# Optimization experiments

Measured on AMD Instinct MI355X. Metric: run time of the kernel, lower is better.

## Reference

```python
import jax, jax.numpy as jnp
import numpy as np

N = 50000      # nodes
E = 800000     # edges (avg degree 16)
D_IN, D_H, D_OUT = 128, 128, 64


def setup_inputs() -> dict:
    key = jax.random.key(0)
    ks = jax.random.split(key, 12)
    s = 0.05  # weight init scale
    return {
        "x": jax.random.normal(ks[0], (N, D_IN), jnp.float32),
        "edge_index": jax.random.randint(ks[1], (2, E), 0, N, dtype=jnp.int64),
        "Wl0": jax.random.normal(ks[2], (D_H, D_IN), jnp.float32) * s,
        "bl0": jax.random.normal(ks[3], (D_H,), jnp.float32) * s,
        "Wr0": jax.random.normal(ks[4], (D_H, D_IN), jnp.float32) * s,
        "Wl1": jax.random.normal(ks[5], (D_H, D_H), jnp.float32) * s,
        "bl1": jax.random.normal(ks[6], (D_H,), jnp.float32) * s,
        "Wr1": jax.random.normal(ks[7], (D_H, D_H), jnp.float32) * s,
        "Wl2": jax.random.normal(ks[8], (D_OUT, D_H), jnp.float32) * s,
        "bl2": jax.random.normal(ks[9], (D_OUT,), jnp.float32) * s,
        "Wr2": jax.random.normal(ks[10], (D_OUT, D_H), jnp.float32) * s,
    }


def _sage_layer(h, src, dst, Wl, bl, Wr):
    # mean aggregation over incoming neighbors: out[i] = mean_{j in N(i)} h[j]
    n = h.shape[0]
    agg = jax.ops.segment_sum(h[src], dst, num_segments=n)          # [N, D]
    deg = jax.ops.segment_sum(jnp.ones((src.shape[0],), h.dtype), dst,
                              num_segments=n)                        # [N]
    mean = agg / jnp.maximum(deg, 1.0)[:, None]  # empty rows -> 0, matches torch_sparse
    # lin_l(agg) + lin_r(self); lin_r has no bias in PyG SAGEConv
    return mean @ Wl.T + bl + h @ Wr.T


def reference(x, edge_index, Wl0, bl0, Wr0, Wl1, bl1, Wr1, Wl2, bl2, Wr2):
    src, dst = edge_index[1], edge_index[0]  # adj row = dst, col = src
    h = jax.nn.relu(_sage_layer(x, src, dst, Wl0, bl0, Wr0))
    h = jax.nn.relu(_sage_layer(h, src, dst, Wl1, bl1, Wr1))
    h = _sage_layer(h, src, dst, Wl2, bl2, Wr2)
    return jax.nn.log_softmax(h, axis=1)
```

## Files before the change

kernel.cpp:

```cpp
#include <hip/hip_runtime.h>
#include <hip/hip_bf16.h>


typedef __attribute__((ext_vector_type(8))) short bf16x8;
typedef __attribute__((ext_vector_type(4))) float f32x4;

#define NPB 128
#define BCAP 2560
#define EPB 8192
#define EPT 32
#define CPAD 16

__device__ __forceinline__ unsigned short f2bf(float f) {
    unsigned int u = __builtin_bit_cast(unsigned int, f);
    u += 0x7fffu + ((u >> 16) & 1u);
    return (unsigned short)(u >> 16);
}
__device__ __forceinline__ float bf2f(unsigned int bits16) {
    return __builtin_bit_cast(float, bits16 << 16);
}


__global__ __launch_bounds__(256) void dist_cast_kernel(const int* __restrict__ dst,
                                                        const int* __restrict__ srcv,
                                                        int* __restrict__ gcnt,
                                                        unsigned int* __restrict__ staging,
                                                        int E, int NBc, int DB, int XB,
                                                        const float* __restrict__ x,
                                                        unsigned short* __restrict__ xbf,
                                                        const float* p0, const float* p1,
                                                        const float* p2, const float* p3,
                                                        const float* p4, const float* p5,
                                                        unsigned short* __restrict__ wbf) {
    __shared__ unsigned int stage[EPB];
    __shared__ int hist[400];
    __shared__ int lstart[400];
    __shared__ int gbase[400];
    __shared__ int scanbuf[256];
    int bid = blockIdx.x;
    int t = threadIdx.x;

    if (bid >= DB && bid < DB + XB) {
        int base = (bid - DB) * 256 + t;
        int stride = XB * 256;
        const float2* x2 = (const float2*)x;
        unsigned int* xo = (unsigned int*)xbf;
#pragma unroll
        for (int k = 0; k < 4; ++k) {
            int idx = base + k * stride;
            float2 v = x2[idx];
            xo[idx] = (unsigned int)f2bf(v.x) | ((unsigned int)f2bf(v.y) << 16);
        }
        return;
    }
    if (bid >= DB + XB) {
        int w = (bid - DB - XB) * 256 + t;
        if (w < 40960) {
            const float* src;
            int local;
            if      (w < 8192)  { src = p0; local = w; }
            else if (w < 16384) { src = p1; local = w - 8192; }
            else if (w < 24576) { src = p2; local = w - 16384; }
            else if (w < 32768) { src = p3; local = w - 24576; }
            else if (w < 36864) { src = p4; local = w - 32768; }
            else                { src = p5; local = w - 36864; }
            float2 v = ((const float2*)src)[local];
            unsigned int p = (unsigned int)f2bf(v.x) | ((unsigned int)f2bf(v.y) << 16);
            ((unsigned int*)wbf)[w] = p;
        }
        return;
    }

    int e0 = bid * EPB;
    unsigned int w[EPT];

    for (int b = t; b < NBc + 1; b += 256) hist[b] = 0;
    __syncthreads();

#pragma unroll
    for (int i = 0; i < EPT; ++i) {
        int e = e0 + i * 256 + t;
        unsigned int word = 0xFFFFFFFFu;
        if (e < E) word = ((unsigned int)dst[e] << 16) | (unsigned int)srcv[e];
        w[i] = word;
        int b = (int)(word >> 23); if (b > NBc) b = NBc;
        atomicAdd(&hist[b], 1);
    }
    __syncthreads();

    int b0 = 2 * t, b1 = 2 * t + 1;
    int h0 = (b0 <= NBc) ? hist[b0] : 0;
    int h1 = (b1 <= NBc) ? hist[b1] : 0;
    int pair = h0 + h1;
    scanbuf[t] = pair;
    __syncthreads();
    for (int off = 1; off < 256; off <<= 1) {
        int v = (t >= off) ? scanbuf[t - off] : 0;
        __syncthreads();
        scanbuf[t] += v;
        __syncthreads();
    }
    int excl = scanbuf[t] - pair;
    if (b0 <= NBc) lstart[b0] = excl;
    if (b1 <= NBc) lstart[b1] = excl + h0;
    __syncthreads();

    for (int b = t; b < NBc; b += 256) {
        int h = hist[b];
        gbase[b] = h ? atomicAdd(&gcnt[b * CPAD], h) : 0;
    }
    for (int b = t; b < NBc + 1; b += 256) hist[b] = lstart[b];
    __syncthreads();

#pragma unroll
    for (int i = 0; i < EPT; ++i) {
        unsigned int word = w[i];
        int b = (int)(word >> 23); if (b > NBc) b = NBc;
        int p = atomicAdd(&hist[b], 1);
        stage[p] = word;
    }
    __syncthreads();

    int total = lstart[NBc];
    for (int i = t; i < total; i += 256) {
        unsigned int word = stage[i];
        int b = (int)(word >> 23);
        int gpos = gbase[b] + (i - lstart[b]);
        staging[(size_t)b * BCAP + gpos] = word;
    }
}


template<int GY>
__device__ __forceinline__ void gemm_body(int mb, int y,
                                          const unsigned short* __restrict__ H,
                                          const unsigned short* __restrict__ Wl,
                                          const unsigned short* __restrict__ Wr,
                                          unsigned short* __restrict__ Cl,
                                          unsigned short* __restrict__ Cr, int N) {
    __shared__ unsigned short clds[4 * 32 * 68];
    const int halfY = GY >> 1;
    const int ldc = GY * 32;
    int wave = threadIdx.x >> 6;
    int lane = threadIdx.x & 63;
    int l15 = lane & 15, quad = lane >> 4;
    bool isL = y < halfY;
    const unsigned short* W = isL ? Wl : Wr;
    unsigned short* Cp = isL ? Cl : Cr;
    int yy = isL ? y : y - halfY;
    int wrow0 = yy * 64;
    int col0 = yy * 64;
    int m0 = mb * 128 + wave * 32;

    int r0 = m0 + l15;      if (r0 > N - 1) r0 = N - 1;
    int r1 = m0 + 16 + l15; if (r1 > N - 1) r1 = N - 1;
    const bf16x8* A0 = (const bf16x8*)(H + (size_t)r0 * 128);
    const bf16x8* A1 = (const bf16x8*)(H + (size_t)r1 * 128);

    f32x4 acc[2][4] = {};
#pragma unroll
    for (int ks = 0; ks < 4; ++ks) {
        int vidx = ks * 4 + quad;
        bf16x8 a0 = A0[vidx];
        bf16x8 a1 = A1[vidx];
#pragma unroll
        for (int j = 0; j < 4; ++j) {
            const bf16x8* B = (const bf16x8*)(W + (size_t)(wrow0 + j * 16 + l15) * 128);
            bf16x8 b = B[vidx];
            acc[0][j] = __builtin_amdgcn_mfma_f32_16x16x32_bf16(a0, b, acc[0][j], 0, 0, 0);
            acc[1][j] = __builtin_amdgcn_mfma_f32_16x16x32_bf16(a1, b, acc[1][j], 0, 0, 0);
        }
    }

    unsigned short* slice = clds + wave * (32 * 68);
#pragma unroll
    for (int i = 0; i < 2; ++i)
#pragma unroll
        for (int j = 0; j < 4; ++j)
#pragma unroll
            for (int r = 0; r < 4; ++r)
                slice[(i * 16 + quad * 4 + r) * 68 + j * 16 + l15] = f2bf(acc[i][j][r]);
    __syncthreads();

    int rlo = lane >> 3, j8 = lane & 7;
#pragma unroll
    for (int pass = 0; pass < 4; ++pass) {
        int row_local = pass * 8 + rlo;
        const unsigned short* p = slice + row_local * 68 + j8 * 8;
        unsigned long long lo = *(const unsigned long long*)(p);
        unsigned long long hi = *(const unsigned long long*)(p + 4);
        int row = m0 + row_local;
        if (row < N) {
            unsigned long long* q = (unsigned long long*)(Cp + (size_t)row * ldc + col0 + j8 * 8);
            q[0] = lo;
            q[1] = hi;
        }
    }
}


__global__ __launch_bounds__(256) void build_gemm_kernel(const unsigned int* __restrict__ staging,
                                                         const int* __restrict__ gcnt,
                                                         int* __restrict__ row_ptr,
                                                         int* __restrict__ adj, int N, int NBc,
                                                         int gemmRows,
                                                         const unsigned short* __restrict__ H,
                                                         const unsigned short* __restrict__ Wl,
                                                         const unsigned short* __restrict__ Wr,
                                                         unsigned short* __restrict__ Cl,
                                                         unsigned short* __restrict__ Cr) {
    __shared__ int hist[NPB];
    __shared__ int scn[NPB];
    __shared__ int wsum[4];
    int bid = blockIdx.x;
    int t = threadIdx.x;

    if (bid >= NBc) {
        int gid = bid - NBc;
        int mb = gid % gemmRows;
        int yy = gid / gemmRows;
        gemm_body<4>(mb, yy, H, Wl, Wr, Cl, Cr, N);
        return;
    }

    int b = bid;
    int n0 = b * NPB;
    int nb = N - n0; if (nb > NPB) nb = NPB;
    int ec = gcnt[b * CPAD];
    const unsigned int* st = staging + (size_t)b * BCAP;

    int a = 0;
    for (int j = t; j < b; j += 256) a += gcnt[j * CPAD];
#pragma unroll
    for (int off = 32; off; off >>= 1) a += __shfl_xor(a, off);
    if ((t & 63) == 0) wsum[t >> 6] = a;
    if (t < NPB) hist[t] = 0;
    __syncthreads();
    int bb = wsum[0] + wsum[1] + wsum[2] + wsum[3];

    for (int i = t; i < ec; i += 256)
        atomicAdd(&hist[(st[i] >> 16) & (NPB - 1)], 1);
    __syncthreads();

    int v = (t < NPB) ? hist[t] : 0;
    if (t < NPB) scn[t] = v;
    __syncthreads();
    for (int off = 1; off < NPB; off <<= 1) {
        int u = (t >= off && t < NPB) ? scn[t - off] : 0;
        __syncthreads();
        if (t < NPB) scn[t] += u;
        __syncthreads();
    }
    if (t < NPB) hist[t] = scn[t] - v;
    if (t < nb) row_ptr[n0 + t] = bb + (scn[t] - v);
    if (b == NBc - 1 && t == 0) row_ptr[N] = bb + ec;
    __syncthreads();

    for (int i = t; i < ec; i += 256) {
        unsigned int pk = st[i];
        int p = atomicAdd(&hist[(pk >> 16) & (NPB - 1)], 1);
        adj[bb + p] = (int)(pk & 0xffffu);
    }
}


template<int GY>
__global__ __launch_bounds__(256) void gemm_mfma_kernel(const unsigned short* __restrict__ H,
                                                        const unsigned short* __restrict__ Wl,
                                                        const unsigned short* __restrict__ Wr,
                                                        unsigned short* __restrict__ Cl,
                                                        unsigned short* __restrict__ Cr,
                                                        int N) {
    gemm_body<GY>(blockIdx.x, blockIdx.y, Wl ? H : H, Wl, Wr, Cl, Cr, N);
}


__global__ __launch_bounds__(256) void agg_relu_kernel(const unsigned short* __restrict__ Cl,
                                                       const unsigned short* __restrict__ Cr,
                                                       const int* __restrict__ row_ptr,
                                                       const int* __restrict__ adj,
                                                       const float* __restrict__ bias,
                                                       unsigned short* __restrict__ hout, int N) {
    int pr = (int)((blockIdx.x * blockDim.x + threadIdx.x) >> 6);
    int lane = threadIdx.x & 63;
    int nodeA = pr * 2;
    if (nodeA >= N) return;
    int nodeB = nodeA + 1;
    bool hasB = nodeB < N;
    int g = lane >> 4, c = lane & 15;
    int begA = row_ptr[nodeA], endA = row_ptr[nodeA + 1];
    int begB = hasB ? row_ptr[nodeB] : 0;
    int endB = hasB ? row_ptr[nodeB + 1] : 0;
    float pA[8] = {}, pB[8] = {};

    int cntA = endA - begA; if (cntA > 64) cntA = 64;
    int cntB = endB - begB; if (cntB > 64) cntB = 64;
    int idxA = (cntA > 0) ? adj[begA + (lane < cntA ? lane : cntA - 1)] : 0;
    int idxB = (cntB > 0) ? adj[begB + (lane < cntB ? lane : cntB - 1)] : 0;
    int c1A = cntA - 1, c1B = cntB - 1;
    int mx = cntA > cntB ? cntA : cntB;
    for (int i = 0; i < mx; i += 16) {
        bool doA = i < cntA, doB = i < cntB;
        bf16x8 vA[4], vB[4];
        float mA[4], mB[4];
        if (doA) {
#pragma unroll
            for (int s = 0; s < 4; ++s) {
                int tt = i + s * 4 + g;
                int src = __shfl(idxA, tt > c1A ? c1A : tt);
                mA[s] = tt < cntA ? 1.f : 0.f;
                vA[s] = ((const bf16x8*)(Cl + (size_t)src * 128))[c];
            }
        }
        if (doB) {
#pragma unroll
            for (int s = 0; s < 4; ++s) {
                int tt = i + s * 4 + g;
                int src = __shfl(idxB, tt > c1B ? c1B : tt);
                mB[s] = tt < cntB ? 1.f : 0.f;
                vB[s] = ((const bf16x8*)(Cl + (size_t)src * 128))[c];
            }
        }
        if (doA) {
#pragma unroll
            for (int s = 0; s < 4; ++s)
#pragma unroll
                for (int k = 0; k < 8; ++k)
                    pA[k] += mA[s] * bf2f((unsigned short)vA[s][k]);
        }
        if (doB) {
#pragma unroll
            for (int s = 0; s < 4; ++s)
#pragma unroll
                for (int k = 0; k < 8; ++k)
                    pB[k] += mB[s] * bf2f((unsigned short)vB[s][k]);
        }
    }
    for (int e = begA + 64; e < endA; e += 64) {
        int cnt = endA - e; if (cnt > 64) cnt = 64;
        int idx = adj[e + (lane < cnt ? lane : cnt - 1)];
        int c1 = cnt - 1;
        for (int i = 0; i < cnt; i += 16) {
#pragma unroll
            for (int s = 0; s < 4; ++s) {
                int tt = i + s * 4 + g;
                int src = __shfl(idx, tt > c1 ? c1 : tt);
                float m = tt < cnt ? 1.f : 0.f;
                bf16x8 v = ((const bf16x8*)(Cl + (size_t)src * 128))[c];
#pragma unroll
                for (int k = 0; k < 8; ++k)
                    pA[k] += m * bf2f((unsigned short)v[k]);
            }
        }
    }
    for (int e = begB + 64; e < endB; e += 64) {
        int cnt = endB - e; if (cnt > 64) cnt = 64;
        int idx = adj[e + (lane < cnt ? lane : cnt - 1)];
        int c1 = cnt - 1;
        for (int i = 0; i < cnt; i += 16) {
#pragma unroll
            for (int s = 0; s < 4; ++s) {
                int tt = i + s * 4 + g;
                int src = __shfl(idx, tt > c1 ? c1 : tt);
                float m = tt < cnt ? 1.f : 0.f;
                bf16x8 v = ((const bf16x8*)(Cl + (size_t)src * 128))[c];
#pragma unroll
                for (int k = 0; k < 8; ++k)
                    pB[k] += m * bf2f((unsigned short)v[k]);
            }
        }
    }

#pragma unroll
    for (int k = 0; k < 8; ++k) {
        pA[k] += __shfl_xor(pA[k], 16);
        pA[k] += __shfl_xor(pA[k], 32);
        pB[k] += __shfl_xor(pB[k], 16);
        pB[k] += __shfl_xor(pB[k], 32);
    }

    int degA = endA - begA, degB = endB - begB;
    float invA = 1.0f / (float)(degA > 1 ? degA : 1);
    float invB = 1.0f / (float)(degB > 1 ? degB : 1);
    bf16x8 svA = ((const bf16x8*)(Cr + (size_t)nodeA * 128))[c];
    bf16x8 svB = hasB ? ((const bf16x8*)(Cr + (size_t)nodeB * 128))[c] : svA;
    float4 b0 = ((const float4*)bias)[2 * c];
    float4 b1 = ((const float4*)bias)[2 * c + 1];
    float bb[8] = {b0.x, b0.y, b0.z, b0.w, b1.x, b1.y, b1.z, b1.w};
    bf16x8 oA, oB;
#pragma unroll
    for (int k = 0; k < 8; ++k) {
        oA[k] = (short)f2bf(fmaxf(pA[k] * invA + bb[k] + bf2f((unsigned short)svA[k]), 0.f));
        oB[k] = (short)f2bf(fmaxf(pB[k] * invB + bb[k] + bf2f((unsigned short)svB[k]), 0.f));
    }
    if (g == 0)
        ((bf16x8*)(hout + (size_t)nodeA * 128))[c] = oA;
    else if (g == 1 && hasB)
        ((bf16x8*)(hout + (size_t)nodeB * 128))[c] = oB;
}


__global__ __launch_bounds__(256) void final_kernel(const unsigned short* __restrict__ Cl2,
                                                    const unsigned short* __restrict__ Cr2,
                                                    const int* __restrict__ row_ptr,
                                                    const int* __restrict__ adj,
                                                    const float* __restrict__ bias,
                                                    float* __restrict__ out, int N) {
    int pr = (int)((blockIdx.x * blockDim.x + threadIdx.x) >> 6);
    int lane = threadIdx.x & 63;
    int nodeA = pr * 2;
    if (nodeA >= N) return;
    int nodeB = nodeA + 1;
    bool hasB = nodeB < N;
    int g = lane >> 3, c = lane & 7;
    int begA = row_ptr[nodeA], endA = row_ptr[nodeA + 1];
    int begB = hasB ? row_ptr[nodeB] : 0;
    int endB = hasB ? row_ptr[nodeB + 1] : 0;
    float pA[8] = {}, pB[8] = {};

    int cntA = endA - begA; if (cntA > 64) cntA = 64;
    int cntB = endB - begB; if (cntB > 64) cntB = 64;
    int idxA = (cntA > 0) ? adj[begA + (lane < cntA ? lane : cntA - 1)] : 0;
    int idxB = (cntB > 0) ? adj[begB + (lane < cntB ? lane : cntB - 1)] : 0;
    int c1A = cntA - 1, c1B = cntB - 1;
    int mx = cntA > cntB ? cntA : cntB;
    for (int i = 0; i < mx; i += 16) {
        bool doA = i < cntA, doB = i < cntB;
        bf16x8 vA[2], vB[2];
        float mA[2], mB[2];
        if (doA) {
#pragma unroll
            for (int s = 0; s < 2; ++s) {
                int tt = i + s * 8 + g;
                int src = __shfl(idxA, tt > c1A ? c1A : tt);
                mA[s] = tt < cntA ? 1.f : 0.f;
                vA[s] = ((const bf16x8*)(Cl2 + (size_t)src * 64))[c];
            }
        }
        if (doB) {
#pragma unroll
            for (int s = 0; s < 2; ++s) {
                int tt = i + s * 8 + g;
                int src = __shfl(idxB, tt > c1B ? c1B : tt);
                mB[s] = tt < cntB ? 1.f : 0.f;
                vB[s] = ((const bf16x8*)(Cl2 + (size_t)src * 64))[c];
            }
        }
        if (doA) {
#pragma unroll
            for (int s = 0; s < 2; ++s)
#pragma unroll
                for (int k = 0; k < 8; ++k)
                    pA[k] += mA[s] * bf2f((unsigned short)vA[s][k]);
        }
        if (doB) {
#pragma unroll
            for (int s = 0; s < 2; ++s)
#pragma unroll
                for (int k = 0; k < 8; ++k)
                    pB[k] += mB[s] * bf2f((unsigned short)vB[s][k]);
        }
    }
    for (int e = begA + 64; e < endA; e += 64) {
        int cnt = endA - e; if (cnt > 64) cnt = 64;
        int idx = adj[e + (lane < cnt ? lane : cnt - 1)];
        int c1 = cnt - 1;
        for (int i = 0; i < cnt; i += 16) {
#pragma unroll
            for (int s = 0; s < 2; ++s) {
                int tt = i + s * 8 + g;
                int src = __shfl(idx, tt > c1 ? c1 : tt);
                float m = tt < cnt ? 1.f : 0.f;
                bf16x8 v = ((const bf16x8*)(Cl2 + (size_t)src * 64))[c];
#pragma unroll
                for (int k = 0; k < 8; ++k)
                    pA[k] += m * bf2f((unsigned short)v[k]);
            }
        }
    }
    for (int e = begB + 64; e < endB; e += 64) {
        int cnt = endB - e; if (cnt > 64) cnt = 64;
        int idx = adj[e + (lane < cnt ? lane : cnt - 1)];
        int c1 = cnt - 1;
        for (int i = 0; i < cnt; i += 16) {
#pragma unroll
            for (int s = 0; s < 2; ++s) {
                int tt = i + s * 8 + g;
                int src = __shfl(idx, tt > c1 ? c1 : tt);
                float m = tt < cnt ? 1.f : 0.f;
                bf16x8 v = ((const bf16x8*)(Cl2 + (size_t)src * 64))[c];
#pragma unroll
                for (int k = 0; k < 8; ++k)
                    pB[k] += m * bf2f((unsigned short)v[k]);
            }
        }
    }

#pragma unroll
    for (int k = 0; k < 8; ++k) {
        pA[k] += __shfl_xor(pA[k], 8);
        pA[k] += __shfl_xor(pA[k], 16);
        pA[k] += __shfl_xor(pA[k], 32);
        pB[k] += __shfl_xor(pB[k], 8);
        pB[k] += __shfl_xor(pB[k], 16);
        pB[k] += __shfl_xor(pB[k], 32);
    }

    int degA = endA - begA, degB = endB - begB;
    float invA = 1.0f / (float)(degA > 1 ? degA : 1);
    float invB = 1.0f / (float)(degB > 1 ? degB : 1);
    bf16x8 svA = ((const bf16x8*)(Cr2 + (size_t)nodeA * 64))[c];
    bf16x8 svB = hasB ? ((const bf16x8*)(Cr2 + (size_t)nodeB * 64))[c] : svA;
    float4 b0 = ((const float4*)bias)[2 * c];
    float4 b1 = ((const float4*)bias)[2 * c + 1];
    float bb[8] = {b0.x, b0.y, b0.z, b0.w, b1.x, b1.y, b1.z, b1.w};
    float uA[8], uB[8];
#pragma unroll
    for (int k = 0; k < 8; ++k) {
        uA[k] = pA[k] * invA + bb[k] + bf2f((unsigned short)svA[k]);
        uB[k] = pB[k] * invB + bb[k] + bf2f((unsigned short)svB[k]);
    }

    float mA_ = uA[0], mB_ = uB[0];
#pragma unroll
    for (int k = 1; k < 8; ++k) { mA_ = fmaxf(mA_, uA[k]); mB_ = fmaxf(mB_, uB[k]); }
#pragma unroll
    for (int off = 1; off < 8; off <<= 1) {
        mA_ = fmaxf(mA_, __shfl_xor(mA_, off));
        mB_ = fmaxf(mB_, __shfl_xor(mB_, off));
    }
    float seA = 0.f, seB = 0.f;
#pragma unroll
    for (int k = 0; k < 8; ++k) { seA += __expf(uA[k] - mA_); seB += __expf(uB[k] - mB_); }
#pragma unroll
    for (int off = 1; off < 8; off <<= 1) {
        seA += __shfl_xor(seA, off);
        seB += __shfl_xor(seB, off);
    }
    float lsA = __logf(seA), lsB = __logf(seB);

    if (g == 0) {
        float4 o0 = {uA[0] - mA_ - lsA, uA[1] - mA_ - lsA, uA[2] - mA_ - lsA, uA[3] - mA_ - lsA};
        float4 o1 = {uA[4] - mA_ - lsA, uA[5] - mA_ - lsA, uA[6] - mA_ - lsA, uA[7] - mA_ - lsA};
        ((float4*)(out + (size_t)nodeA * 64))[2 * c] = o0;
        ((float4*)(out + (size_t)nodeA * 64))[2 * c + 1] = o1;
    } else if (g == 1 && hasB) {
        float4 o0 = {uB[0] - mB_ - lsB, uB[1] - mB_ - lsB, uB[2] - mB_ - lsB, uB[3] - mB_ - lsB};
        float4 o1 = {uB[4] - mB_ - lsB, uB[5] - mB_ - lsB, uB[6] - mB_ - lsB, uB[7] - mB_ - lsB};
        ((float4*)(out + (size_t)nodeB * 64))[2 * c] = o0;
        ((float4*)(out + (size_t)nodeB * 64))[2 * c + 1] = o1;
    }
}


extern "C" void kernel_launch(void* const* d_in, const int* in_sizes, int n_in,
                              void* d_out, int out_size, void* d_ws, size_t ws_size,
                              hipStream_t stream) {
    const float* x   = (const float*)d_in[0];
    const int*   ei  = (const int*)d_in[1];
    const float* Wl0 = (const float*)d_in[2];
    const float* bl0 = (const float*)d_in[3];
    const float* Wr0 = (const float*)d_in[4];
    const float* Wl1 = (const float*)d_in[5];
    const float* bl1 = (const float*)d_in[6];
    const float* Wr1 = (const float*)d_in[7];
    const float* Wl2 = (const float*)d_in[8];
    const float* bl2 = (const float*)d_in[9];
    const float* Wr2 = (const float*)d_in[10];
    float* out = (float*)d_out;

    const int N  = in_sizes[0] / 128;
    const int E  = in_sizes[1] / 2;
    const int NB = (N + NPB - 1) / NPB;

    char* ws = (char*)d_ws;
    auto alloc = [&](size_t bytes) {
        char* p = ws;
        ws += (bytes + 255) & ~(size_t)255;
        return p;
    };
    int*   row_ptr    = (int*)alloc((size_t)(N + 1) * 4);
    int*   adj        = (int*)alloc((size_t)E * 4);
    int*   gcnt      = (int*)alloc((size_t)NB * CPAD * 4);
    unsigned int* staging = (unsigned int*)alloc((size_t)NB * BCAP * 4);
    unsigned short* xbf = (unsigned short*)alloc((size_t)N * 128 * 2);
    unsigned short* wbf = (unsigned short*)alloc((size_t)81920 * 2);
    unsigned short* Cl  = (unsigned short*)alloc((size_t)N * 128 * 2);
    unsigned short* Cr  = (unsigned short*)alloc((size_t)N * 128 * 2);
    unsigned short* hA  = (unsigned short*)alloc((size_t)N * 128 * 2);
    unsigned short* hB  = (unsigned short*)alloc((size_t)N * 128 * 2);

    const int* dstp = ei;
    const int* srcp = ei + E;

    unsigned short* wl0 = wbf;
    unsigned short* wr0 = wbf + 16384;
    unsigned short* wl1 = wbf + 32768;
    unsigned short* wr1 = wbf + 49152;
    unsigned short* wl2 = wbf + 65536;
    unsigned short* wr2 = wbf + 73728;

    dim3 blk(256);
    int DB = (E + EPB - 1) / EPB;
    int XB = (N * 64) / (256 * 4);
    int gemmRows = (N + 127) / 128;
    int pairBlocks = (((N + 1) / 2) * 64 + 255) / 256;

    hipMemsetAsync(gcnt, 0, (size_t)NB * CPAD * 4, stream);
    dist_cast_kernel<<<DB + XB + 160, blk, 0, stream>>>(dstp, srcp, gcnt, staging, E, NB,
                                                        DB, XB, x, xbf,
                                                        Wl0, Wr0, Wl1, Wr1, Wl2, Wr2, wbf);
    build_gemm_kernel<<<NB + gemmRows * 4, blk, 0, stream>>>(staging, gcnt, row_ptr, adj,
                                                             N, NB, gemmRows, xbf, wl0, wr0,
                                                             Cl, Cr);
    agg_relu_kernel<<<pairBlocks, blk, 0, stream>>>(Cl, Cr, row_ptr, adj, bl0, hA, N);
    gemm_mfma_kernel<4><<<dim3(gemmRows, 4), blk, 0, stream>>>(hA, wl1, wr1, Cl, Cr, N);
    agg_relu_kernel<<<pairBlocks, blk, 0, stream>>>(Cl, Cr, row_ptr, adj, bl1, hB, N);
    gemm_mfma_kernel<2><<<dim3(gemmRows, 2), blk, 0, stream>>>(hB, wl2, wr2, Cl, Cr, N);
    final_kernel<<<pairBlocks, blk, 0, stream>>>(Cl, Cr, row_ptr, adj, bl2, out, N);
}
```

Baseline: 273.3 us.

## Store 128-wide features in column-sliced layout and aggregate per slice

The GEMM epilogue for layers 0 and 1 now writes the neighbor-projected features in a sliced layout of eight [N,16] column slices instead of row-major [N,128]. A new aggregation kernel assigns each block one slice, and each lane pair gathers 32-byte rows per neighbor. This shrinks the per-slice gather working set so it stays cache-resident and improves L2 locality of random neighbor reads. The following GEMM reads its A operand from the sliced layout. It trades coalesced wide row reads for more blocks, eight passes over adjacency, and an extra __syncthreads in the GEMM.

```diff
diff --git a/kernel.cpp b/kernel.cpp
--- a/kernel.cpp
+++ b/kernel.cpp
@@ -131,7 +131,7 @@
 }
 
 
-template<int GY>
+template<int GY, int ASL, int CSL>
 __device__ __forceinline__ void gemm_body(int mb, int y,
                                           const unsigned short* __restrict__ H,
                                           const unsigned short* __restrict__ Wl,
@@ -154,15 +154,20 @@
 
     int r0 = m0 + l15;      if (r0 > N - 1) r0 = N - 1;
     int r1 = m0 + 16 + l15; if (r1 > N - 1) r1 = N - 1;
-    const bf16x8* A0 = (const bf16x8*)(H + (size_t)r0 * 128);
-    const bf16x8* A1 = (const bf16x8*)(H + (size_t)r1 * 128);
 
     f32x4 acc[2][4] = {};
 #pragma unroll
     for (int ks = 0; ks < 4; ++ks) {
         int vidx = ks * 4 + quad;
-        bf16x8 a0 = A0[vidx];
-        bf16x8 a1 = A1[vidx];
+        bf16x8 a0, a1;
+        if constexpr (ASL) {
+            const unsigned short* base = H + (size_t)(vidx >> 1) * N * 16 + (vidx & 1) * 8;
+            a0 = *(const bf16x8*)(base + (size_t)r0 * 16);
+            a1 = *(const bf16x8*)(base + (size_t)r1 * 16);
+        } else {
+            a0 = ((const bf16x8*)(H + (size_t)r0 * 128))[vidx];
+            a1 = ((const bf16x8*)(H + (size_t)r1 * 128))[vidx];
+        }
 #pragma unroll
         for (int j = 0; j < 4; ++j) {
             const bf16x8* B = (const bf16x8*)(W + (size_t)(wrow0 + j * 16 + l15) * 128);
@@ -182,20 +187,40 @@
                 slice[(i * 16 + quad * 4 + r) * 68 + j * 16 + l15] = f2bf(acc[i][j][r]);
     __syncthreads();
 
-    int rlo = lane >> 3, j8 = lane & 7;
-#pragma unroll
-    for (int pass = 0; pass < 4; ++pass) {
-        int row_local = pass * 8 + rlo;
-        const unsigned short* p = slice + row_local * 68 + j8 * 8;
-        unsigned long long lo = *(const unsigned long long*)(p);
-        unsigned long long hi = *(const unsigned long long*)(p + 4);
-        int row = m0 + row_local;
+    if (CSL && isL) {
+        int nodeLocal = lane >> 1, hf = lane & 1;
+        int row = m0 + nodeLocal;
+        int s0 = col0 >> 4;
         if (row < N) {
-            unsigned long long* q = (unsigned long long*)(Cp + (size_t)row * ldc + col0 + j8 * 8);
-            q[0] = lo;
-            q[1] = hi;
-        }
-    }
+#pragma unroll
+            for (int sl = 0; sl < 4; ++sl) {
+                const unsigned short* p = slice + nodeLocal * 68 + sl * 16 + hf * 8;
+                unsigned long long lo = *(const unsigned long long*)(p);
+                unsigned long long hi = *(const unsigned long long*)(p + 4);
+                unsigned long long* q =
+                    (unsigned long long*)(Cl + ((size_t)(s0 + sl) * N + row) * 16 + hf * 8);
+                q[0] = lo;
+                q[1] = hi;
+            }
+        }
+    } else {
+        int rlo = lane >> 3, j8 = lane & 7;
+#pragma unroll
+        for (int pass = 0; pass < 4; ++pass) {
+            int row_local = pass * 8 + rlo;
+            const unsigned short* p = slice + row_local * 68 + j8 * 8;
+            unsigned long long lo = *(const unsigned long long*)(p);
+            unsigned long long hi = *(const unsigned long long*)(p + 4);
+            int row = m0 + row_local;
+            if (row < N) {
+                unsigned long long* q =
+                    (unsigned long long*)(Cp + (size_t)row * ldc + col0 + j8 * 8);
+                q[0] = lo;
+                q[1] = hi;
+            }
+        }
+    }
+    __syncthreads();
 }
 
 
@@ -217,9 +242,7 @@
 
     if (bid >= NBc) {
         int gid = bid - NBc;
-        int mb = gid % gemmRows;
-        int yy = gid / gemmRows;
-        gemm_body<4>(mb, yy, H, Wl, Wr, Cl, Cr, N);
+        gemm_body<4, 0, 1>(gid % gemmRows, gid / gemmRows, H, Wl, Wr, Cl, Cr, N);
         return;
     }
 
@@ -264,139 +287,69 @@
 }
 
 
-template<int GY>
+template<int GY, int ASL, int CSL>
 __global__ __launch_bounds__(256) void gemm_mfma_kernel(const unsigned short* __restrict__ H,
                                                         const unsigned short* __restrict__ Wl,
                                                         const unsigned short* __restrict__ Wr,
                                                         unsigned short* __restrict__ Cl,
                                                         unsigned short* __restrict__ Cr,
                                                         int N) {
-    gemm_body<GY>(blockIdx.x, blockIdx.y, Wl ? H : H, Wl, Wr, Cl, Cr, N);
-}
-
-
-__global__ __launch_bounds__(256) void agg_relu_kernel(const unsigned short* __restrict__ Cl,
-                                                       const unsigned short* __restrict__ Cr,
-                                                       const int* __restrict__ row_ptr,
-                                                       const int* __restrict__ adj,
-                                                       const float* __restrict__ bias,
-                                                       unsigned short* __restrict__ hout, int N) {
-    int pr = (int)((blockIdx.x * blockDim.x + threadIdx.x) >> 6);
+    gemm_body<GY, ASL, CSL>(blockIdx.x, blockIdx.y, H, Wl, Wr, Cl, Cr, N);
+}
+
+
+__global__ __launch_bounds__(256) void agg_sliced_kernel(const unsigned short* __restrict__ Cls,
+                                                         const unsigned short* __restrict__ Cr,
+                                                         const int* __restrict__ row_ptr,
+                                                         const int* __restrict__ adj,
+                                                         const float* __restrict__ bias,
+                                                         unsigned short* __restrict__ houts,
+                                                         int N) {
+    int s = blockIdx.x & 7;
+    int nb = blockIdx.x >> 3;
+    int wave = threadIdx.x >> 6;
     int lane = threadIdx.x & 63;
-    int nodeA = pr * 2;
-    if (nodeA >= N) return;
-    int nodeB = nodeA + 1;
-    bool hasB = nodeB < N;
-    int g = lane >> 4, c = lane & 15;
-    int begA = row_ptr[nodeA], endA = row_ptr[nodeA + 1];
-    int begB = hasB ? row_ptr[nodeB] : 0;
-    int endB = hasB ? row_ptr[nodeB + 1] : 0;
-    float pA[8] = {}, pB[8] = {};
-
-    int cntA = endA - begA; if (cntA > 64) cntA = 64;
-    int cntB = endB - begB; if (cntB > 64) cntB = 64;
-    int idxA = (cntA > 0) ? adj[begA + (lane < cntA ? lane : cntA - 1)] : 0;
-    int idxB = (cntB > 0) ? adj[begB + (lane < cntB ? lane : cntB - 1)] : 0;
-    int c1A = cntA - 1, c1B = cntB - 1;
-    int mx = cntA > cntB ? cntA : cntB;
-    for (int i = 0; i < mx; i += 16) {
-        bool doA = i < cntA, doB = i < cntB;
-        bf16x8 vA[4], vB[4];
-        float mA[4], mB[4];
-        if (doA) {
-#pragma unroll
-            for (int s = 0; s < 4; ++s) {
-                int tt = i + s * 4 + g;
-                int src = __shfl(idxA, tt > c1A ? c1A : tt);
-                mA[s] = tt < cntA ? 1.f : 0.f;
-                vA[s] = ((const bf16x8*)(Cl + (size_t)src * 128))[c];
-            }
-        }
-        if (doB) {
-#pragma unroll
-            for (int s = 0; s < 4; ++s) {
-                int tt = i + s * 4 + g;
-                int src = __shfl(idxB, tt > c1B ? c1B : tt);
-                mB[s] = tt < cntB ? 1.f : 0.f;
-                vB[s] = ((const bf16x8*)(Cl + (size_t)src * 128))[c];
-            }
-        }
-        if (doA) {
-#pragma unroll
-            for (int s = 0; s < 4; ++s)
-#pragma unroll
-                for (int k = 0; k < 8; ++k)
-                    pA[k] += mA[s] * bf2f((unsigned short)vA[s][k]);
-        }
-        if (doB) {
-#pragma unroll
-            for (int s = 0; s < 4; ++s)
-#pragma unroll
-                for (int k = 0; k < 8; ++k)
-                    pB[k] += mB[s] * bf2f((unsigned short)vB[s][k]);
-        }
-    }
-    for (int e = begA + 64; e < endA; e += 64) {
-        int cnt = endA - e; if (cnt > 64) cnt = 64;
-        int idx = adj[e + (lane < cnt ? lane : cnt - 1)];
-        int c1 = cnt - 1;
-        for (int i = 0; i < cnt; i += 16) {
-#pragma unroll
-            for (int s = 0; s < 4; ++s) {
-                int tt = i + s * 4 + g;
-                int src = __shfl(idx, tt > c1 ? c1 : tt);
-                float m = tt < cnt ? 1.f : 0.f;
-                bf16x8 v = ((const bf16x8*)(Cl + (size_t)src * 128))[c];
-#pragma unroll
-                for (int k = 0; k < 8; ++k)
-                    pA[k] += m * bf2f((unsigned short)v[k]);
-            }
-        }
-    }
-    for (int e = begB + 64; e < endB; e += 64) {
-        int cnt = endB - e; if (cnt > 64) cnt = 64;
-        int idx = adj[e + (lane < cnt ? lane : cnt - 1)];
-        int c1 = cnt - 1;
-        for (int i = 0; i < cnt; i += 16) {
-#pragma unroll
-            for (int s = 0; s < 4; ++s) {
-                int tt = i + s * 4 + g;
-                int src = __shfl(idx, tt > c1 ? c1 : tt);
-                float m = tt < cnt ? 1.f : 0.f;
-                bf16x8 v = ((const bf16x8*)(Cl + (size_t)src * 128))[c];
-#pragma unroll
-                for (int k = 0; k < 8; ++k)
-                    pB[k] += m * bf2f((unsigned short)v[k]);
-            }
-        }
-    }
-
-#pragma unroll
-    for (int k = 0; k < 8; ++k) {
-        pA[k] += __shfl_xor(pA[k], 16);
-        pA[k] += __shfl_xor(pA[k], 32);
-        pB[k] += __shfl_xor(pB[k], 16);
-        pB[k] += __shfl_xor(pB[k], 32);
-    }
-
-    int degA = endA - begA, degB = endB - begB;
-    float invA = 1.0f / (float)(degA > 1 ? degA : 1);
-    float invB = 1.0f / (float)(degB > 1 ? degB : 1);
-    bf16x8 svA = ((const bf16x8*)(Cr + (size_t)nodeA * 128))[c];
-    bf16x8 svB = hasB ? ((const bf16x8*)(Cr + (size_t)nodeB * 128))[c] : svA;
-    float4 b0 = ((const float4*)bias)[2 * c];
-    float4 b1 = ((const float4*)bias)[2 * c + 1];
+    int node = nb * 128 + wave * 32 + (lane >> 1);
+    int half = lane & 1;
+    if (node >= N) return;
+    int beg = row_ptr[node], end = row_ptr[node + 1];
+    const unsigned short* tab = Cls + (size_t)s * N * 16 + half * 8;
+
+    float acc[8] = {};
+    int e = beg;
+    for (; e + 4 <= end; e += 4) {
+        int i0 = adj[e], i1 = adj[e + 1], i2 = adj[e + 2], i3 = adj[e + 3];
+        bf16x8 v0 = *(const bf16x8*)(tab + (size_t)i0 * 16);
+        bf16x8 v1 = *(const bf16x8*)(tab + (size_t)i1 * 16);
+        bf16x8 v2 = *(const bf16x8*)(tab + (size_t)i2 * 16);
+        bf16x8 v3 = *(const bf16x8*)(tab + (size_t)i3 * 16);
+#pragma unroll
+        for (int k = 0; k < 8; ++k) acc[k] += bf2f((unsigned short)v0[k]);
+#pragma unroll
+        for (int k = 0; k < 8; ++k) acc[k] += bf2f((unsigned short)v1[k]);
+#pragma unroll
+        for (int k = 0; k < 8; ++k) acc[k] += bf2f((unsigned short)v2[k]);
+#pragma unroll
+        for (int k = 0; k < 8; ++k) acc[k] += bf2f((unsigned short)v3[k]);
+    }
+    for (; e < end; ++e) {
+        int i0 = adj[e];
+        bf16x8 v0 = *(const bf16x8*)(tab + (size_t)i0 * 16);
+#pragma unroll
+        for (int k = 0; k < 8; ++k) acc[k] += bf2f((unsigned short)v0[k]);
+    }
+
+    int deg = end - beg;
+    float inv = 1.0f / (float)(deg > 1 ? deg : 1);
+    bf16x8 sv = *(const bf16x8*)(Cr + (size_t)node * 128 + s * 16 + half * 8);
+    float4 b0 = ((const float4*)bias)[s * 4 + half * 2];
+    float4 b1 = ((const float4*)bias)[s * 4 + half * 2 + 1];
     float bb[8] = {b0.x, b0.y, b0.z, b0.w, b1.x, b1.y, b1.z, b1.w};
-    bf16x8 oA, oB;
-#pragma unroll
-    for (int k = 0; k < 8; ++k) {
-        oA[k] = (short)f2bf(fmaxf(pA[k] * invA + bb[k] + bf2f((unsigned short)svA[k]), 0.f));
-        oB[k] = (short)f2bf(fmaxf(pB[k] * invB + bb[k] + bf2f((unsigned short)svB[k]), 0.f));
-    }
-    if (g == 0)
-        ((bf16x8*)(hout + (size_t)nodeA * 128))[c] = oA;
-    else if (g == 1 && hasB)
-        ((bf16x8*)(hout + (size_t)nodeB * 128))[c] = oB;
+    bf16x8 o;
+#pragma unroll
+    for (int k = 0; k < 8; ++k)
+        o[k] = (short)f2bf(fmaxf(acc[k] * inv + bb[k] + bf2f((unsigned short)sv[k]), 0.f));
+    *(bf16x8*)(houts + ((size_t)s * N + node) * 16 + half * 8) = o;
 }
 
 
@@ -430,35 +383,35 @@
         float mA[2], mB[2];
         if (doA) {
 #pragma unroll
-            for (int s = 0; s < 2; ++s) {
-                int tt = i + s * 8 + g;
+            for (int ss = 0; ss < 2; ++ss) {
+                int tt = i + ss * 8 + g;
                 int src = __shfl(idxA, tt > c1A ? c1A : tt);
-                mA[s] = tt < cntA ? 1.f : 0.f;
-                vA[s] = ((const bf16x8*)(Cl2 + (size_t)src * 64))[c];
+                mA[ss] = tt < cntA ? 1.f : 0.f;
+                vA[ss] = ((const bf16x8*)(Cl2 + (size_t)src * 64))[c];
             }
         }
         if (doB) {
 #pragma unroll
-            for (int s = 0; s < 2; ++s) {
-                int tt = i + s * 8 + g;
+            for (int ss = 0; ss < 2; ++ss) {
+                int tt = i + ss * 8 + g;
                 int src = __shfl(idxB, tt > c1B ? c1B : tt);
-                mB[s] = tt < cntB ? 1.f : 0.f;
-                vB[s] = ((const bf16x8*)(Cl2 + (size_t)src * 64))[c];
+                mB[ss] = tt < cntB ? 1.f : 0.f;
+                vB[ss] = ((const bf16x8*)(Cl2 + (size_t)src * 64))[c];
             }
         }
         if (doA) {
 #pragma unroll
-            for (int s = 0; s < 2; ++s)
+            for (int ss = 0; ss < 2; ++ss)
 #pragma unroll
                 for (int k = 0; k < 8; ++k)
-                    pA[k] += mA[s] * bf2f((unsigned short)vA[s][k]);
+                    pA[k] += mA[ss] * bf2f((unsigned short)vA[ss][k]);
         }
         if (doB) {
 #pragma unroll
-            for (int s = 0; s < 2; ++s)
+            for (int ss = 0; ss < 2; ++ss)
 #pragma unroll
                 for (int k = 0; k < 8; ++k)
-                    pB[k] += mB[s] * bf2f((unsigned short)vB[s][k]);
+                    pB[k] += mB[ss] * bf2f((unsigned short)vB[ss][k]);
         }
     }
     for (int e = begA + 64; e < endA; e += 64) {
@@ -467,8 +420,8 @@
         int c1 = cnt - 1;
         for (int i = 0; i < cnt; i += 16) {
 #pragma unroll
-            for (int s = 0; s < 2; ++s) {
-                int tt = i + s * 8 + g;
+            for (int ss = 0; ss < 2; ++ss) {
+                int tt = i + ss * 8 + g;
                 int src = __shfl(idx, tt > c1 ? c1 : tt);
                 float m = tt < cnt ? 1.f : 0.f;
                 bf16x8 v = ((const bf16x8*)(Cl2 + (size_t)src * 64))[c];
@@ -484,8 +437,8 @@
         int c1 = cnt - 1;
         for (int i = 0; i < cnt; i += 16) {
 #pragma unroll
-            for (int s = 0; s < 2; ++s) {
-                int tt = i + s * 8 + g;
+            for (int ss = 0; ss < 2; ++ss) {
+                int tt = i + ss * 8 + g;
                 int src = __shfl(idx, tt > c1 ? c1 : tt);
                 float m = tt < cnt ? 1.f : 0.f;
                 bf16x8 v = ((const bf16x8*)(Cl2 + (size_t)src * 64))[c];
@@ -604,6 +557,7 @@
     int DB = (E + EPB - 1) / EPB;
     int XB = (N * 64) / (256 * 4);
     int gemmRows = (N + 127) / 128;
+    int aggSlBlocks = ((N + 127) / 128) * 8;
     int pairBlocks = (((N + 1) / 2) * 64 + 255) / 256;
 
     hipMemsetAsync(gcnt, 0, (size_t)NB * CPAD * 4, stream);
@@ -613,9 +567,9 @@
     build_gemm_kernel<<<NB + gemmRows * 4, blk, 0, stream>>>(staging, gcnt, row_ptr, adj,
                                                              N, NB, gemmRows, xbf, wl0, wr0,
                                                              Cl, Cr);
-    agg_relu_kernel<<<pairBlocks, blk, 0, stream>>>(Cl, Cr, row_ptr, adj, bl0, hA, N);
-    gemm_mfma_kernel<4><<<dim3(gemmRows, 4), blk, 0, stream>>>(hA, wl1, wr1, Cl, Cr, N);
-    agg_relu_kernel<<<pairBlocks, blk, 0, stream>>>(Cl, Cr, row_ptr, adj, bl1, hB, N);
-    gemm_mfma_kernel<2><<<dim3(gemmRows, 2), blk, 0, stream>>>(hB, wl2, wr2, Cl, Cr, N);
+    agg_sliced_kernel<<<aggSlBlocks, blk, 0, stream>>>(Cl, Cr, row_ptr, adj, bl0, hA, N);
+    gemm_mfma_kernel<4, 1, 1><<<dim3(gemmRows, 4), blk, 0, stream>>>(hA, wl1, wr1, Cl, Cr, N);
+    agg_sliced_kernel<<<aggSlBlocks, blk, 0, stream>>>(Cl, Cr, row_ptr, adj, bl1, hB, N);
+    gemm_mfma_kernel<2, 1, 0><<<dim3(gemmRows, 2), blk, 0, stream>>>(hB, wl2, wr2, Cl, Cr, N);
     final_kernel<<<pairBlocks, blk, 0, stream>>>(Cl, Cr, row_ptr, adj, bl2, out, N);
 }
```

Result: slower. 284.1 us (+4.0%).
